# Optimization experiments

Measured on AMD Instinct MI355X. Metric: run time of the kernel, lower is better.

The kernel has to match this reference:

```python
import jax, jax.numpy as jnp
import numpy as np

D_MODEL = 128
SEQ_LEN = 2048
WINDOW = 64
BATCH = 32


def setup_inputs() -> dict:
    key = jax.random.key(0)
    ks = jax.random.split(key, 6)
    scale = 1.0 / np.sqrt(D_MODEL)
    return {
        "x": jax.random.normal(ks[0], (BATCH, D_MODEL, SEQ_LEN), dtype=jnp.float32),
        "Wq": jax.random.normal(ks[1], (D_MODEL, D_MODEL), dtype=jnp.float32) * scale,
        "bq": jnp.zeros((D_MODEL,), dtype=jnp.float32),
        "Wk": jax.random.normal(ks[2], (D_MODEL, D_MODEL), dtype=jnp.float32) * scale,
        "bk": jnp.zeros((D_MODEL,), dtype=jnp.float32),
        "Wv": jax.random.normal(ks[3], (D_MODEL, D_MODEL), dtype=jnp.float32) * scale,
        "bv": jnp.zeros((D_MODEL,), dtype=jnp.float32),
        "Wo": jax.random.normal(ks[4], (D_MODEL, D_MODEL), dtype=jnp.float32) * scale,
        "bo": jnp.zeros((D_MODEL,), dtype=jnp.float32),
        "pos_bias": jax.random.normal(ks[5], (SEQ_LEN, SEQ_LEN), dtype=jnp.float32) * 0.02,
    }


def reference(x, Wq, bq, Wk, bk, Wv, bv, Wo, bo, pos_bias):
    # x: [N, C, L] -> [N, L, C]  (in_proj Rearrange)
    xt = jnp.swapaxes(x, 1, 2)
    L = xt.shape[1]

    q = xt @ Wq + bq  # [N, L, d]
    k = xt @ Wk + bk
    v = xt @ Wv + bv

    # AFT-Local positional bias: w_{t,t'} = pos_bias if |t-t'| < s else 0
    idx = jnp.arange(L)
    local_mask = (jnp.abs(idx[:, None] - idx[None, :]) < WINDOW).astype(xt.dtype)
    pb = pos_bias[:L, :L] * local_mask  # [L, L]

    # numerically stable exponentials (AFT paper / labml formulation)
    exp_k = jnp.exp(k - jnp.max(k, axis=1, keepdims=True))          # [N, L, d]
    exp_pb = jnp.exp(pb - jnp.max(pb, axis=1, keepdims=True))       # [L, L]

    num = jnp.einsum('ij,njd->nid', exp_pb, exp_k * v)  # [N, L, d]
    den = jnp.einsum('ij,njd->nid', exp_pb, exp_k)      # [N, L, d]

    y = jax.nn.sigmoid(q) * num / den
    out = y @ Wo + bo  # output projection

    # out_proj Rearrange: [N, L, C] -> [N, C, L]
    return jnp.swapaxes(out, 1, 2)
```

## Files before the change

kernel.cpp:

```cpp
#include <hip/hip_runtime.h>
#include <math.h>

#define NB 32
#define DM 128
#define SL 2048
#define WIN 64
#define NT  (SL / 16)
#define PADF 4
#define PADB 6
#define NTP (NT + PADF + PADB)
#define YST 132

typedef __attribute__((ext_vector_type(8))) short bf16x8;
typedef __attribute__((ext_vector_type(4))) float f32x4;

__device__ inline ushort bf16_rne(float f) {
    union { float f; unsigned u; } v; v.f = f;
    unsigned u = v.u;
    return (ushort)((u + 0x7FFFu + ((u >> 16) & 1u)) >> 16);
}
__device__ inline float bf16_to_f(ushort h) {
    union { unsigned u; float f; } v; v.u = ((unsigned)h) << 16;
    return v.f;
}


__global__ __launch_bounds__(512) void setup_kernel(
    const float* __restrict__ Wq, const float* __restrict__ Wk,
    const float* __restrict__ Wv, const float* __restrict__ Wo,
    const float* __restrict__ pos_bias,
    ushort* __restrict__ Wh, ushort* __restrict__ Wl,
    ushort* __restrict__ WB)
{
    const int b = blockIdx.x;
    const int tid = threadIdx.x;
    if (b < 128) {
        const int id = b;
        const int mat = id >> 5;
        const int ct = (id & 31) >> 2, ks = id & 3;
        const int lane = tid >> 3, j = tid & 7;
        const int k = ks * 32 + (lane >> 4) * 8 + j;
        const int col = ct * 16 + (lane & 15);
        const float* W = (mat == 0) ? Wq : ((mat == 1) ? Wk : ((mat == 2) ? Wv : Wo));
        float w = W[k * DM + col];
        ushort h = bf16_rne(w);
        Wh[(size_t)id * 512 + tid] = h;
        Wl[(size_t)id * 512 + tid] = bf16_rne(w - bf16_to_f(h));
    } else {
        const int idx = b - 128;
        const int it = idx >> 1;
        const int half = idx & 1;
        const int i0 = it * 16;
        const int tend = half * 1280 + 1280;
        for (int t = half * 1280 + tid; t < tend; t += 512) {
            const int ks = t >> 9;
            const int lane = (t >> 3) & 63;
            const int jj = t & 7;
            const int m = lane & 15;
            const int k = ks * 32 + ((lane >> 4) << 3) + jj;
            const int i = i0 + m;
            const int j = i0 - 64 + k;
            const int rel = k - 64 - m;
            float val = 0.f;
            if (rel > -WIN && rel < WIN && j >= 0 && j < SL)
                val = __expf(pos_bias[(size_t)i * SL + j]) - 1.f;
            WB[(size_t)it * 2560 + t] = bf16_rne(val);
        }
    }
}

__global__ __launch_bounds__(512, 4) void qkv_kernel(
    const float* __restrict__ x,
    const ushort* __restrict__ Wh, const ushort* __restrict__ Wl,
    const float* __restrict__ bq, const float* __restrict__ bk,
    const float* __restrict__ bv,
    ushort* __restrict__ sqh, ushort* __restrict__ ekTF, ushort* __restrict__ ekvTF,
    float* __restrict__ Pk, float* __restrict__ Pkv)
{
    __shared__ ushort Ah[64 * 128];
    __shared__ ushort Al[64 * 128];
    const int n = blockIdx.y, bx = blockIdx.x, l0 = bx * 64;
    const int tid = threadIdx.x;
    const int wave = tid >> 6;
    const int lane = tid & 63;

    if (bx < 10) {
        const int jt_p = (bx < PADF) ? bx : (NT + bx);
        const size_t zb = ((size_t)n * NTP + jt_p) * 2048 + (size_t)tid * 4;
        ushort4 z; z.x = 0; z.y = 0; z.z = 0; z.w = 0;
        *(ushort4*)&ekTF [zb] = z;
        *(ushort4*)&ekvTF[zb] = z;
    }

    const bf16x8* WhV = (const bf16x8*)Wh;
    const bf16x8* WlV = (const bf16x8*)Wl;

    bf16x8 bh0[3], bl0[3];
    #pragma unroll
    for (int m = 0; m < 3; ++m) {
        const int fi = ((m * 8 + wave) * 4 + 0) * 64 + lane;
        bh0[m] = WhV[fi];
        bl0[m] = WlV[fi];
    }

    {
        const int lo = lane;
        const int cq = wave;
        const int l  = l0 + lo;
        for (int cc = 0; cc < 4; ++cc) {
            const int c0 = cc * 32 + cq * 4;
            float xv[4]; ushort hh[4], ll[4];
            #pragma unroll
            for (int u = 0; u < 4; ++u)
                xv[u] = x[((size_t)n * DM + c0 + u) * SL + l];
            #pragma unroll
            for (int u = 0; u < 4; ++u) {
                hh[u] = bf16_rne(xv[u]);
                ll[u] = bf16_rne(xv[u] - bf16_to_f(hh[u]));
            }
            const int idx = ((lo >> 4) * 4 + (c0 >> 5)) * 512
                          + (((c0 >> 3) & 3) * 16 + (lo & 15)) * 8 + (c0 & 7);
            ushort4 hv; hv.x = hh[0]; hv.y = hh[1]; hv.z = hh[2]; hv.w = hh[3];
            ushort4 lv; lv.x = ll[0]; lv.y = ll[1]; lv.z = ll[2]; lv.w = ll[3];
            *(ushort4*)&Ah[idx] = hv;
            *(ushort4*)&Al[idx] = lv;
        }
    }
    __syncthreads();

    const int dcol = lane & 15;
    const int d = wave * 16 + dcol;

    f32x4 acc[3][4];
    {
        const float b0 = bq[d], b1 = bk[d], b2 = bv[d];
        #pragma unroll
        for (int lt = 0; lt < 4; ++lt) {
            acc[0][lt] = (f32x4){b0, b0, b0, b0};
            acc[1][lt] = (f32x4){b1, b1, b1, b1};
            acc[2][lt] = (f32x4){b2, b2, b2, b2};
        }
    }

    #pragma unroll
    for (int ks = 0; ks < 4; ++ks) {
        bf16x8 bh[3], bl[3];
        if (ks == 0) {
            #pragma unroll
            for (int m = 0; m < 3; ++m) { bh[m] = bh0[m]; bl[m] = bl0[m]; }
        } else {
            #pragma unroll
            for (int m = 0; m < 3; ++m) {
                const int fi = ((m * 8 + wave) * 4 + ks) * 64 + lane;
                bh[m] = WhV[fi];
                bl[m] = WlV[fi];
            }
        }
        #pragma unroll
        for (int lt = 0; lt < 4; ++lt) {
            const bf16x8 ah = *(const bf16x8*)&Ah[((lt * 4 + ks) * 64 + lane) * 8];
            const bf16x8 al = *(const bf16x8*)&Al[((lt * 4 + ks) * 64 + lane) * 8];
            #pragma unroll
            for (int m = 0; m < 3; ++m) {
                acc[m][lt] = __builtin_amdgcn_mfma_f32_16x16x32_bf16(
                    ah, bh[m], acc[m][lt], 0, 0, 0);
                acc[m][lt] = __builtin_amdgcn_mfma_f32_16x16x32_bf16(
                    al, bh[m], acc[m][lt], 0, 0, 0);
                acc[m][lt] = __builtin_amdgcn_mfma_f32_16x16x32_bf16(
                    ah, bl[m], acc[m][lt], 0, 0, 0);
            }
        }
    }

    const int lrow0 = (lane >> 4) * 4;
    float psk = 0.f, pskv = 0.f;
    #pragma unroll
    for (int lt = 0; lt < 4; ++lt) {
        const f32x4 q4 = acc[0][lt];
        const f32x4 k4 = acc[1][lt];
        const f32x4 v4 = acc[2][lt];
        ushort eh[4], zh[4];
        #pragma unroll
        for (int r = 0; r < 4; ++r) {
            const int l = l0 + lt * 16 + lrow0 + r;
            const float e = __expf(k4[r]);
            const float z = e * v4[r];
            const float s = 1.f / (1.f + __expf(-q4[r]));
            sqh[((size_t)n * SL + l) * DM + d] = (ushort)(s * 65535.f + 0.5f);
            eh[r] = bf16_rne(e);
            zh[r] = bf16_rne(z);
            psk  += e;
            pskv += z;
        }
        const size_t tb = ((size_t)n * NTP + PADF + ((l0 + lt * 16) >> 4)) * 2048
                        + (size_t)d * 16 + lrow0;
        ushort4 ev; ev.x = eh[0]; ev.y = eh[1]; ev.z = eh[2]; ev.w = eh[3];
        ushort4 zv; zv.x = zh[0]; zv.y = zh[1]; zv.z = zh[2]; zv.w = zh[3];
        *(ushort4*)&ekTF [tb] = ev;
        *(ushort4*)&ekvTF[tb] = zv;
    }
    {
        float a = psk, b = pskv;
        a += __shfl_xor(a, 16, 64); a += __shfl_xor(a, 32, 64);
        b += __shfl_xor(b, 16, 64); b += __shfl_xor(b, 32, 64);
        if (lane < 16) {
            const size_t o = ((size_t)n * 32 + bx) * DM + d;
            Pk [o] = a;
            Pkv[o] = b;
        }
    }
}

__global__ __launch_bounds__(256, 4) void band_out_kernel(
    const ushort* __restrict__ ekTF, const ushort* __restrict__ ekvTF,
    const ushort* __restrict__ WB,
    const float* __restrict__ Pk, const float* __restrict__ Pkv,
    const ushort* __restrict__ sqg,
    const ushort* __restrict__ Wh, const ushort* __restrict__ Wl,
    const float* __restrict__ bo, float* __restrict__ out)
{
    __shared__ __align__(16) union {
        float ylds[64 * YST];
        float ot[128 * 65];
    } u;
    __shared__ float SkL[DM], SkvL[DM];

    const int bid = blockIdx.x;
    const int xcd = bid & 7;
    const int slot = bid >> 3;
    const int nsub = slot >> 5;
    const int itg  = slot & 31;
    const int n = xcd * 4 + nsub;
    const int wave = threadIdx.x >> 6;
    const int lane = threadIdx.x & 63;
    const int it = itg * 4 + wave;
    const int i0 = it * 16;
    const int l0 = itg * 64;

    const int dcol = lane & 15;
    const int jgrp8 = (lane >> 4) << 3;

    const bf16x8* WBv = (const bf16x8*)(WB + (size_t)it * 2560);
    bf16x8 aWB[5];
    #pragma unroll
    for (int ks = 0; ks < 5; ++ks) aWB[ks] = WBv[ks * 64 + lane];

    {
        const int tdd = threadIdx.x & 127;
        const float* P = (threadIdx.x < 128) ? Pk : Pkv;
        float s = 0.f;
        #pragma unroll
        for (int seg = 0; seg < 32; ++seg)
            s += P[((size_t)n * 32 + seg) * DM + tdd];
        if (threadIdx.x < 128) SkL[tdd] = s; else SkvL[tdd] = s;
    }
    __syncthreads();

    f32x4 den[8], num[8];
    #pragma unroll
    for (int dt = 0; dt < 8; ++dt) {
        const float sk = SkL [dt * 16 + dcol];
        const float sv = SkvL[dt * 16 + dcol];
        den[dt] = (f32x4){sk, sk, sk, sk};
        num[dt] = (f32x4){sv, sv, sv, sv};
    }

    const size_t lsel = (size_t)(lane >> 5) * 2048 + (size_t)((lane >> 4) & 1) * 8
                      + (size_t)dcol * 16;
    #pragma unroll
    for (int ks = 0; ks < 5; ++ks) {
        const bf16x8 a = aWB[ks];
        const size_t tb = ((size_t)n * NTP + it + 2 * ks) * 2048 + lsel;
        #pragma unroll
        for (int dt = 0; dt < 8; ++dt) {
            const size_t rbase = tb + (size_t)dt * 256;
            const bf16x8 bden = *(const bf16x8*)(ekTF  + rbase);
            const bf16x8 bnum = *(const bf16x8*)(ekvTF + rbase);
            den[dt] = __builtin_amdgcn_mfma_f32_16x16x32_bf16(a, bden, den[dt], 0, 0, 0);
            num[dt] = __builtin_amdgcn_mfma_f32_16x16x32_bf16(a, bnum, num[dt], 0, 0, 0);
        }
    }

    const int irow0 = (lane >> 4) << 2;
    #pragma unroll
    for (int dt = 0; dt < 8; ++dt) {
        const int d = dt * 16 + dcol;
        #pragma unroll
        for (int r = 0; r < 4; ++r) {
            const int i = i0 + irow0 + r;
            const float s = (float)sqg[((size_t)n * SL + i) * DM + d] * (1.f / 65535.f);
            const float y = s * num[dt][r] / den[dt][r];
            u.ylds[(wave * 16 + irow0 + r) * YST + d] = y;
        }
    }

    float af[4][8];
    {
        const int arow = wave * 16 + (lane & 15);
        #pragma unroll
        for (int ks = 0; ks < 4; ++ks) {
            const int base = arow * YST + ks * 32 + jgrp8;
            const float4 a0 = *(const float4*)&u.ylds[base];
            const float4 a1 = *(const float4*)&u.ylds[base + 4];
            af[ks][0] = a0.x; af[ks][1] = a0.y; af[ks][2] = a0.z; af[ks][3] = a0.w;
            af[ks][4] = a1.x; af[ks][5] = a1.y; af[ks][6] = a1.z; af[ks][7] = a1.w;
        }
    }
    __syncthreads();

    bf16x8 yh[4], yl[4];
    #pragma unroll
    for (int ks = 0; ks < 4; ++ks) {
        #pragma unroll
        for (int t = 0; t < 8; ++t) {
            const float v = af[ks][t];
            const ushort h = bf16_rne(v);
            yh[ks][t] = (short)h;
            yl[ks][t] = (short)bf16_rne(v - bf16_to_f(h));
        }
    }

    f32x4 acc[8];
    #pragma unroll
    for (int ct = 0; ct < 8; ++ct) {
        const float b0 = bo[ct * 16 + dcol];
        acc[ct] = (f32x4){b0, b0, b0, b0};
    }

    const bf16x8* WhV = (const bf16x8*)Wh;
    const bf16x8* WlV = (const bf16x8*)Wl;
    #pragma unroll
    for (int ks = 0; ks < 4; ++ks) {
        #pragma unroll
        for (int ct = 0; ct < 8; ++ct) {
            const int fi = ((24 + ct) * 4 + ks) * 64 + lane;
            const bf16x8 bh = WhV[fi];
            const bf16x8 bl = WlV[fi];
            acc[ct] = __builtin_amdgcn_mfma_f32_16x16x32_bf16(yh[ks], bh, acc[ct], 0, 0, 0);
            acc[ct] = __builtin_amdgcn_mfma_f32_16x16x32_bf16(yl[ks], bh, acc[ct], 0, 0, 0);
            acc[ct] = __builtin_amdgcn_mfma_f32_16x16x32_bf16(yh[ks], bl, acc[ct], 0, 0, 0);
        }
    }

    #pragma unroll
    for (int ct = 0; ct < 8; ++ct) {
        const int c = ct * 16 + dcol;
        #pragma unroll
        for (int r = 0; r < 4; ++r)
            u.ot[c * 65 + wave * 16 + irow0 + r] = acc[ct][r];
    }
    __syncthreads();

    const int tid = threadIdx.x;
    #pragma unroll
    for (int rep = 0; rep < 32; ++rep) {
        const int e = rep * 256 + tid;
        const int c = e >> 6, l = e & 63;
        out[((size_t)n * DM + c) * SL + l0 + l] = u.ot[c * 65 + l];
    }
}

extern "C" void kernel_launch(void* const* d_in, const int* in_sizes, int n_in,
                              void* d_out, int out_size, void* d_ws, size_t ws_size,
                              hipStream_t stream)
{
    const float* x        = (const float*)d_in[0];
    const float* Wq       = (const float*)d_in[1];
    const float* bq       = (const float*)d_in[2];
    const float* Wk       = (const float*)d_in[3];
    const float* bk       = (const float*)d_in[4];
    const float* Wv       = (const float*)d_in[5];
    const float* bv       = (const float*)d_in[6];
    const float* Wo       = (const float*)d_in[7];
    const float* bo       = (const float*)d_in[8];
    const float* pos_bias = (const float*)d_in[9];
    float* out = (float*)d_out;

    const size_t NLD = (size_t)NB * SL * DM;
    ushort* sqh   = (ushort*)d_ws;
    ushort* ekTF  = sqh   + NLD;
    ushort* ekvTF = ekTF  + (size_t)NB * NTP * 2048;
    ushort* WB    = ekvTF + (size_t)NB * NTP * 2048;
    float*  Pk    = (float*)(WB + (size_t)128 * 2560);
    float*  Pkv   = Pk   + (size_t)NB * 32 * DM;
    ushort* Wh    = (ushort*)(Pkv + (size_t)NB * 32 * DM);
    ushort* Wl    = Wh + (size_t)4 * DM * DM;

    setup_kernel   <<<dim3(384),     512, 0, stream>>>(Wq, Wk, Wv, Wo, pos_bias,
                                                       Wh, Wl, WB);
    qkv_kernel     <<<dim3(32, NB),  512, 0, stream>>>(x, Wh, Wl, bq, bk, bv,
                                                       sqh, ekTF, ekvTF, Pk, Pkv);
    band_out_kernel<<<dim3(NB * 32), 256, 0, stream>>>(ekTF, ekvTF, WB, Pk, Pkv, sqh,
                                                       Wh, Wl, bo, out);
}
```

Before: 162.1 us.

## Halve QKV tile to 32 rows, doubling blocks, and use fast reciprocals

Shrinks the qkv_kernel sequence tile from 64 to 32 positions, so the grid doubles to 64 segments per batch. LDS use per block is halved and the occupancy hint is raised, which is meant to improve latency hiding. The partial-sum buffers and their reduction in band_out_kernel are resized to match. It also replaces divisions with the hardware rcp instruction, uses truncation for the high part of the bf16 split, and vectorises the x staging to 8-wide stores. In exchange, weight fragments are reloaded per block with less reuse, and there is a small precision change from rcp and truncation.

Result: no change. 160.0 us (-1.3%).

```diff
diff --git a/kernel.cpp b/kernel.cpp
--- a/kernel.cpp
+++ b/kernel.cpp
@@ -10,8 +10,10 @@
 #define PADB 6
 #define NTP (NT + PADF + PADB)
 #define YST 132
+#define NSEG 64
 
 typedef __attribute__((ext_vector_type(8))) short bf16x8;
+typedef __attribute__((ext_vector_type(8))) unsigned short u16x8;
 typedef __attribute__((ext_vector_type(4))) float f32x4;
 
 __device__ inline ushort bf16_rne(float f) {
@@ -22,6 +24,10 @@
 __device__ inline float bf16_to_f(ushort h) {
     union { unsigned u; float f; } v; v.u = ((unsigned)h) << 16;
     return v.f;
+}
+__device__ inline ushort bf16_hi_trunc(float f) {
+    union { float f; unsigned u; } v; v.f = f;
+    return (ushort)(v.u >> 16);
 }
 
 
@@ -69,7 +75,7 @@
     }
 }
 
-__global__ __launch_bounds__(512, 4) void qkv_kernel(
+__global__ __launch_bounds__(512, 6) void qkv_kernel(
     const float* __restrict__ x,
     const ushort* __restrict__ Wh, const ushort* __restrict__ Wl,
     const float* __restrict__ bq, const float* __restrict__ bk,
@@ -77,9 +83,9 @@
     ushort* __restrict__ sqh, ushort* __restrict__ ekTF, ushort* __restrict__ ekvTF,
     float* __restrict__ Pk, float* __restrict__ Pkv)
 {
-    __shared__ ushort Ah[64 * 128];
-    __shared__ ushort Al[64 * 128];
-    const int n = blockIdx.y, bx = blockIdx.x, l0 = bx * 64;
+    __shared__ ushort Ah[32 * 128];
+    __shared__ ushort Al[32 * 128];
+    const int n = blockIdx.y, bx = blockIdx.x, l0 = bx * 32;
     const int tid = threadIdx.x;
     const int wave = tid >> 6;
     const int lane = tid & 63;
@@ -92,72 +98,57 @@
         *(ushort4*)&ekvTF[zb] = z;
     }
 
-    const bf16x8* WhV = (const bf16x8*)Wh;
-    const bf16x8* WlV = (const bf16x8*)Wl;
-
-    bf16x8 bh0[3], bl0[3];
-    #pragma unroll
-    for (int m = 0; m < 3; ++m) {
-        const int fi = ((m * 8 + wave) * 4 + 0) * 64 + lane;
-        bh0[m] = WhV[fi];
-        bl0[m] = WlV[fi];
-    }
-
-    {
-        const int lo = lane;
-        const int cq = wave;
+    {
+        const int lo = tid & 31;
+        const int cq = tid >> 5;
         const int l  = l0 + lo;
-        for (int cc = 0; cc < 4; ++cc) {
-            const int c0 = cc * 32 + cq * 4;
-            float xv[4]; ushort hh[4], ll[4];
-            #pragma unroll
-            for (int u = 0; u < 4; ++u)
-                xv[u] = x[((size_t)n * DM + c0 + u) * SL + l];
-            #pragma unroll
-            for (int u = 0; u < 4; ++u) {
-                hh[u] = bf16_rne(xv[u]);
-                ll[u] = bf16_rne(xv[u] - bf16_to_f(hh[u]));
-            }
-            const int idx = ((lo >> 4) * 4 + (c0 >> 5)) * 512
-                          + (((c0 >> 3) & 3) * 16 + (lo & 15)) * 8 + (c0 & 7);
-            ushort4 hv; hv.x = hh[0]; hv.y = hh[1]; hv.z = hh[2]; hv.w = hh[3];
-            ushort4 lv; lv.x = ll[0]; lv.y = ll[1]; lv.z = ll[2]; lv.w = ll[3];
-            *(ushort4*)&Ah[idx] = hv;
-            *(ushort4*)&Al[idx] = lv;
-        }
+        const int c0 = cq * 8;
+        float xv[8];
+        #pragma unroll
+        for (int u = 0; u < 8; ++u)
+            xv[u] = x[((size_t)n * DM + c0 + u) * SL + l];
+        u16x8 hv, lv;
+        #pragma unroll
+        for (int u = 0; u < 8; ++u) {
+            const ushort h = bf16_hi_trunc(xv[u]);
+            hv[u] = h;
+            lv[u] = bf16_rne(xv[u] - bf16_to_f(h));
+        }
+        const int lt = lo >> 4, m = lo & 15;
+        const int ks = cq >> 2, oct = cq & 3;
+        const int idx = ((lt * 4 + ks) * 64 + oct * 16 + m) * 8;
+        *(u16x8*)&Ah[idx] = hv;
+        *(u16x8*)&Al[idx] = lv;
     }
     __syncthreads();
 
     const int dcol = lane & 15;
     const int d = wave * 16 + dcol;
 
-    f32x4 acc[3][4];
+    f32x4 acc[3][2];
     {
         const float b0 = bq[d], b1 = bk[d], b2 = bv[d];
         #pragma unroll
-        for (int lt = 0; lt < 4; ++lt) {
+        for (int lt = 0; lt < 2; ++lt) {
             acc[0][lt] = (f32x4){b0, b0, b0, b0};
             acc[1][lt] = (f32x4){b1, b1, b1, b1};
             acc[2][lt] = (f32x4){b2, b2, b2, b2};
         }
     }
 
+    const bf16x8* WhV = (const bf16x8*)Wh;
+    const bf16x8* WlV = (const bf16x8*)Wl;
     #pragma unroll
     for (int ks = 0; ks < 4; ++ks) {
         bf16x8 bh[3], bl[3];
-        if (ks == 0) {
-            #pragma unroll
-            for (int m = 0; m < 3; ++m) { bh[m] = bh0[m]; bl[m] = bl0[m]; }
-        } else {
-            #pragma unroll
-            for (int m = 0; m < 3; ++m) {
-                const int fi = ((m * 8 + wave) * 4 + ks) * 64 + lane;
-                bh[m] = WhV[fi];
-                bl[m] = WlV[fi];
-            }
-        }
-        #pragma unroll
-        for (int lt = 0; lt < 4; ++lt) {
+        #pragma unroll
+        for (int m = 0; m < 3; ++m) {
+            const int fi = ((m * 8 + wave) * 4 + ks) * 64 + lane;
+            bh[m] = WhV[fi];
+            bl[m] = WlV[fi];
+        }
+        #pragma unroll
+        for (int lt = 0; lt < 2; ++lt) {
             const bf16x8 ah = *(const bf16x8*)&Ah[((lt * 4 + ks) * 64 + lane) * 8];
             const bf16x8 al = *(const bf16x8*)&Al[((lt * 4 + ks) * 64 + lane) * 8];
             #pragma unroll
@@ -175,7 +166,7 @@
     const int lrow0 = (lane >> 4) * 4;
     float psk = 0.f, pskv = 0.f;
     #pragma unroll
-    for (int lt = 0; lt < 4; ++lt) {
+    for (int lt = 0; lt < 2; ++lt) {
         const f32x4 q4 = acc[0][lt];
         const f32x4 k4 = acc[1][lt];
         const f32x4 v4 = acc[2][lt];
@@ -185,14 +176,14 @@
             const int l = l0 + lt * 16 + lrow0 + r;
             const float e = __expf(k4[r]);
             const float z = e * v4[r];
-            const float s = 1.f / (1.f + __expf(-q4[r]));
+            const float s = fminf(__builtin_amdgcn_rcpf(1.f + __expf(-q4[r])), 1.f);
             sqh[((size_t)n * SL + l) * DM + d] = (ushort)(s * 65535.f + 0.5f);
             eh[r] = bf16_rne(e);
             zh[r] = bf16_rne(z);
             psk  += e;
             pskv += z;
         }
-        const size_t tb = ((size_t)n * NTP + PADF + ((l0 + lt * 16) >> 4)) * 2048
+        const size_t tb = ((size_t)n * NTP + PADF + (bx * 2 + lt)) * 2048
                         + (size_t)d * 16 + lrow0;
         ushort4 ev; ev.x = eh[0]; ev.y = eh[1]; ev.z = eh[2]; ev.w = eh[3];
         ushort4 zv; zv.x = zh[0]; zv.y = zh[1]; zv.z = zh[2]; zv.w = zh[3];
@@ -204,7 +195,7 @@
         a += __shfl_xor(a, 16, 64); a += __shfl_xor(a, 32, 64);
         b += __shfl_xor(b, 16, 64); b += __shfl_xor(b, 32, 64);
         if (lane < 16) {
-            const size_t o = ((size_t)n * 32 + bx) * DM + d;
+            const size_t o = ((size_t)n * NSEG + bx) * DM + d;
             Pk [o] = a;
             Pkv[o] = b;
         }
@@ -250,8 +241,8 @@
         const float* P = (threadIdx.x < 128) ? Pk : Pkv;
         float s = 0.f;
         #pragma unroll
-        for (int seg = 0; seg < 32; ++seg)
-            s += P[((size_t)n * 32 + seg) * DM + tdd];
+        for (int seg = 0; seg < NSEG; ++seg)
+            s += P[((size_t)n * NSEG + seg) * DM + tdd];
         if (threadIdx.x < 128) SkL[tdd] = s; else SkvL[tdd] = s;
     }
     __syncthreads();
@@ -289,12 +280,12 @@
         for (int r = 0; r < 4; ++r) {
             const int i = i0 + irow0 + r;
             const float s = (float)sqg[((size_t)n * SL + i) * DM + d] * (1.f / 65535.f);
-            const float y = s * num[dt][r] / den[dt][r];
+            const float y = s * num[dt][r] * __builtin_amdgcn_rcpf(den[dt][r]);
             u.ylds[(wave * 16 + irow0 + r) * YST + d] = y;
         }
     }
 
-    float af[4][8];
+    bf16x8 yh[4], yl[4];
     {
         const int arow = wave * 16 + (lane & 15);
         #pragma unroll
@@ -302,23 +293,18 @@
             const int base = arow * YST + ks * 32 + jgrp8;
             const float4 a0 = *(const float4*)&u.ylds[base];
             const float4 a1 = *(const float4*)&u.ylds[base + 4];
-            af[ks][0] = a0.x; af[ks][1] = a0.y; af[ks][2] = a0.z; af[ks][3] = a0.w;
-            af[ks][4] = a1.x; af[ks][5] = a1.y; af[ks][6] = a1.z; af[ks][7] = a1.w;
+            float af[8];
+            af[0] = a0.x; af[1] = a0.y; af[2] = a0.z; af[3] = a0.w;
+            af[4] = a1.x; af[5] = a1.y; af[6] = a1.z; af[7] = a1.w;
+            #pragma unroll
+            for (int t = 0; t < 8; ++t) {
+                const ushort h = bf16_hi_trunc(af[t]);
+                yh[ks][t] = (short)h;
+                yl[ks][t] = (short)bf16_rne(af[t] - bf16_to_f(h));
+            }
         }
     }
     __syncthreads();
-
-    bf16x8 yh[4], yl[4];
-    #pragma unroll
-    for (int ks = 0; ks < 4; ++ks) {
-        #pragma unroll
-        for (int t = 0; t < 8; ++t) {
-            const float v = af[ks][t];
-            const ushort h = bf16_rne(v);
-            yh[ks][t] = (short)h;
-            yl[ks][t] = (short)bf16_rne(v - bf16_to_f(h));
-        }
-    }
 
     f32x4 acc[8];
     #pragma unroll
@@ -382,14 +368,14 @@
     ushort* ekvTF = ekTF  + (size_t)NB * NTP * 2048;
     ushort* WB    = ekvTF + (size_t)NB * NTP * 2048;
     float*  Pk    = (float*)(WB + (size_t)128 * 2560);
-    float*  Pkv   = Pk   + (size_t)NB * 32 * DM;
-    ushort* Wh    = (ushort*)(Pkv + (size_t)NB * 32 * DM);
+    float*  Pkv   = Pk   + (size_t)NB * NSEG * DM;
+    ushort* Wh    = (ushort*)(Pkv + (size_t)NB * NSEG * DM);
     ushort* Wl    = Wh + (size_t)4 * DM * DM;
 
-    setup_kernel   <<<dim3(384),     512, 0, stream>>>(Wq, Wk, Wv, Wo, pos_bias,
-                                                       Wh, Wl, WB);
-    qkv_kernel     <<<dim3(32, NB),  512, 0, stream>>>(x, Wh, Wl, bq, bk, bv,
-                                                       sqh, ekTF, ekvTF, Pk, Pkv);
-    band_out_kernel<<<dim3(NB * 32), 256, 0, stream>>>(ekTF, ekvTF, WB, Pk, Pkv, sqh,
-                                                       Wh, Wl, bo, out);
-}
+    setup_kernel   <<<dim3(384),      512, 0, stream>>>(Wq, Wk, Wv, Wo, pos_bias,
+                                                        Wh, Wl, WB);
+    qkv_kernel     <<<dim3(NSEG, NB), 512, 0, stream>>>(x, Wh, Wl, bq, bk, bv,
+                                                        sqh, ekTF, ekvTF, Pk, Pkv);
+    band_out_kernel<<<dim3(NB * 32),  256, 0, stream>>>(ekTF, ekvTF, WB, Pk, Pkv, sqh,
+                                                        Wh, Wl, bo, out);
+}
```
